# Performance work log

Hardware: AMD Instinct MI355X
Metric: run time of the kernel (lower is better)

The kernel has to match this reference:

```python
import jax, jax.numpy as jnp
import numpy as np

MASK_FILL = -987654321.0


def rotate_every_two(x):
    # pairs (x0, x1) -> (-x1, x0), interleaved back along last dim
    x1 = x[..., 0::2]
    x2 = x[..., 1::2]
    return jnp.stack((-x2, x1), axis=-1).reshape(x.shape)


def setup_inputs() -> dict:
    key = jax.random.key(0)
    ks = jax.random.split(key, 6)
    b, n, dim = 64, 197, 768
    heads, dim_head = 12, 64
    inner = heads * dim_head
    x = jax.random.normal(ks[0], (b, n, dim), dtype=jnp.float32)
    pos_emb = jax.random.normal(ks[1], (1, n, dim_head), dtype=jnp.float32)
    w_qkv = jax.random.normal(ks[2], (dim, 3 * inner), dtype=jnp.float32) * (dim ** -0.5)
    scale = jnp.full((heads,), dim_head ** -0.5, dtype=jnp.float32)
    w_out = jax.random.normal(ks[3], (inner, dim), dtype=jnp.float32) * (inner ** -0.5)
    b_out = jnp.zeros((dim,), dtype=jnp.float32)
    return {"x": x, "pos_emb": pos_emb, "w_qkv": w_qkv, "scale": scale,
            "w_out": w_out, "b_out": b_out}


def reference(x, pos_emb, w_qkv, scale, w_out, b_out):
    b, n, dim = x.shape
    h = scale.shape[0]
    qkv = x @ w_qkv                         # [b, n, 3*inner]
    q, k, v = jnp.split(qkv, 3, axis=-1)
    dh = q.shape[-1] // h
    to_heads = lambda t: t.reshape(b, n, h, dh).transpose(0, 2, 1, 3)  # bhnd
    q, k, v = to_heads(q), to_heads(k), to_heads(v)

    # RoPE: pos_emb [1, n, (2 * dh/2)] -> sin/cos [n, dh/2] -> interleave to [n, dh]
    sc = pos_emb[0].reshape(n, 2, dh // 2)
    sin = jnp.repeat(sc[:, 0], 2, axis=-1)  # [n, dh]
    cos = jnp.repeat(sc[:, 1], 2, axis=-1)
    q = q * cos + rotate_every_two(q) * sin
    k = k * cos + rotate_every_two(k) * sin

    # per-head learnable scale
    dots = jnp.einsum('bhid,bhjd->bhij', q, k) * scale[None, :, None, None]
    # diagonal (LSA) mask
    eye = jnp.eye(n, dtype=bool)
    dots = jnp.where(eye, MASK_FILL, dots)

    attn = jax.nn.softmax(dots, axis=-1)
    out = jnp.einsum('bhij,bhjd->bhid', attn, v)
    out = out.transpose(0, 2, 1, 3).reshape(b, n, h * dh)
    return out @ w_out + b_out
```

## Files before the change

kernel.cpp:

```cpp
#include <hip/hip_runtime.h>
#include <math.h>

#define MASK_FILL_F (-987654321.0f)

typedef unsigned short u16;
typedef unsigned int   u32;

constexpr int Bb   = 64;
constexpr int Ntok = 197;
constexpr int Dim  = 768;
constexpr int Heads= 12;
constexpr int Dh   = 64;
constexpr int Nq3  = 2304;
constexpr int Rows = 12608;
constexpr int Mpad = 12672;

using f32x4  = __attribute__((ext_vector_type(4))) float;
using bf16x8 = __attribute__((ext_vector_type(8))) short;

__device__ __forceinline__ u16 f2bf(float f) {
  u32 u = __float_as_uint(f);
  u = (u + 0x7fffu + ((u >> 16) & 1u)) >> 16;
  return (u16)u;
}

__device__ __forceinline__ void stage16(const void* gp, void* lp) {
  __builtin_amdgcn_global_load_lds(
      (const __attribute__((address_space(1))) u32*)gp,
      (__attribute__((address_space(3))) u32*)lp, 16, 0, 0);
}

__device__ __forceinline__ int sigma6(int M) {
  return (M & 0x23) | (((M >> 3) & 1) << 4) | (((M >> 2) & 1) << 3) |
         (((M >> 4) & 1) << 2);
}

constexpr int NB_CVT = (Rows * Dim / 4 + 255) / 256;
constexpr int NB_TQ  = (Nq3 / 32) * (Dim / 32);
constexpr int NB_TO  = (Dim / 32) * (Dim / 32);

__global__ __launch_bounds__(256) void prep(
    const float* __restrict__ x, u16* __restrict__ xb,
    const float* __restrict__ w_qkv, u16* __restrict__ wqkvT,
    const float* __restrict__ w_out, u16* __restrict__ woutT)
{
  __shared__ float t[32][33];
  const int bid = blockIdx.x, tid = threadIdx.x;

  if (bid < NB_CVT) {
    const int i = bid * 256 + tid;
    if (i < Rows * Dim / 4) {
      const float4 v = *(const float4*)&x[(size_t)i * 4];
      ushort4 u;
      u.x = f2bf(v.x); u.y = f2bf(v.y); u.z = f2bf(v.z); u.w = f2bf(v.w);
      *(ushort4*)&xb[(size_t)i * 4] = u;
    }
    return;
  }

  const float* in; u16* out; int R, C, c0, r0;
  if (bid < NB_CVT + NB_TQ) {
    const int b2 = bid - NB_CVT;
    in = w_qkv; out = wqkvT; R = Dim; C = Nq3;
    c0 = (b2 % (Nq3 / 32)) * 32; r0 = (b2 / (Nq3 / 32)) * 32;
  } else {
    const int b3 = bid - NB_CVT - NB_TQ;
    in = w_out; out = woutT; R = Dim; C = Dim;
    c0 = (b3 % (Dim / 32)) * 32; r0 = (b3 / (Dim / 32)) * 32;
  }
  const int tx = tid & 31, ty = tid >> 5;
#pragma unroll
  for (int rr = ty; rr < 32; rr += 8)
    t[rr][tx] = in[(size_t)(r0 + rr) * C + c0 + tx];
  __syncthreads();
#pragma unroll
  for (int cc = ty; cc < 32; cc += 8)
    out[(size_t)(c0 + cc) * R + r0 + tx] = f2bf(t[tx][cc]);
}

constexpr int Kc  = 768;
constexpr int NKT = Kc / 64;
#define KTC(x) ((x) < NKT ? (x) : (NKT - 1))

#define BARM()  asm volatile("s_barrier" ::: "memory")
#define VMW4()  asm volatile("s_waitcnt vmcnt(4)" ::: "memory")
#define LGKM0() asm volatile("s_waitcnt lgkmcnt(0)" ::: "memory")

#define STGA(chunk, kt, BUF) \
  stage16(Ag + (size_t)(m0 + (chunk) * 8 + srow) * Kc + (kt) * 64 + scol, \
          &As[BUF][(chunk) * 512])
#define STGB(chunk, kt, BUF) \
  stage16(Bg + (size_t)(n0 + (chunk) * 8 + srow) * Kc + (kt) * 64 + scol, \
          &Bs[BUF][(chunk) * 512])

#define RDA(BUF, MH) \
  _Pragma("unroll") for (int m_ = 0; m_ < 4; ++m_) \
  _Pragma("unroll") for (int k_ = 0; k_ < 2; ++k_) \
    af[m_][k_] = *(const bf16x8*)&As[BUF][(wr * 128 + (MH) * 64 + m_ * 16 + tx) * 64 \
                                          + (((k_ * 4 + qd) ^ sx) * 8)];
#define RDB(BUF, NH, BFR) \
  _Pragma("unroll") for (int n_ = 0; n_ < 2; ++n_) \
  _Pragma("unroll") for (int k_ = 0; k_ < 2; ++k_) \
    BFR[n_][k_] = *(const bf16x8*)&Bs[BUF][(wc * 64 + (NH) * 32 + n_ * 16 + tx) * 64 \
                                           + (((k_ * 4 + qd) ^ sx) * 8)];

#define MM(MH, NH, BFR) \
  __builtin_amdgcn_s_setprio(1); \
  _Pragma("unroll") for (int m_ = 0; m_ < 4; ++m_) \
  _Pragma("unroll") for (int n_ = 0; n_ < 2; ++n_) \
  _Pragma("unroll") for (int k_ = 0; k_ < 2; ++k_) \
    acc[(MH) * 4 + m_][(NH) * 2 + n_] = __builtin_amdgcn_mfma_f32_16x16x32_bf16( \
        af[m_][k_], BFR[n_][k_], acc[(MH) * 4 + m_][(NH) * 2 + n_], 0, 0, 0); \
  __builtin_amdgcn_s_setprio(0);

template<int TN>
__global__ __launch_bounds__(512, 2) void gemm8p(
    const u16* __restrict__ Ag, const u16* __restrict__ Bg,
    u16* __restrict__ Cb, int Nn, int nwg,
    const float* __restrict__ pe)
{
  __shared__ u16 As[2][256 * 64];
  __shared__ u16 Bs[2][256 * 64];

  const int tid = threadIdx.x, lane = tid & 63, w = tid >> 6;

  const int orig = blockIdx.x;
  const int q8 = nwg >> 3, r8 = nwg & 7;
  const int xcd = orig & 7, sub = orig >> 3;
  const int wgid = (xcd < r8 ? xcd * (q8 + 1) : r8 * (q8 + 1) + (xcd - r8) * q8) + sub;
  const int tm = wgid / TN, tn = wgid % TN;
  const int m0 = tm * 256, n0 = tn * 256;

  const int wr = w >> 2, wc = w & 3;
  const int tx = lane & 15, qd = lane >> 4, sx = tx & 7;

  const int srow = lane >> 3;
  const int scol = ((lane & 7) ^ srow) * 8;
  const int b0 = (w >> 1) * 8 + (w & 1) * 2;

  STGA(w, 0, 0);        STGA(16 + w, 0, 0);
  STGB(b0 + 4, 0, 0);   STGB(b0 + 5, 0, 0);
  STGA(8 + w, 0, 0);    STGA(24 + w, 0, 0);
  STGB(b0, 0, 0);       STGB(b0 + 1, 0, 0);
  STGA(w, 1, 1);        STGA(16 + w, 1, 1);
  STGB(b0 + 4, 1, 1);   STGB(b0 + 5, 1, 1);
  VMW4();
  BARM();

  f32x4  acc[8][4] = {};
  bf16x8 af[4][2], bf0[2][2], bf1[2][2];

#pragma unroll 1
  for (int i = 0; i < NKT / 2; ++i) {
    const int u = 2 * i;
    RDA(0, 0); RDB(0, 0, bf0); RDB(0, 1, bf1);
    STGA(8 + w, u + 1, 1); STGA(24 + w, u + 1, 1);
    STGB(b0, u + 1, 1);    STGB(b0 + 1, u + 1, 1);
    LGKM0(); BARM();
    MM(0, 0, bf0); MM(0, 1, bf1);
    RDA(0, 1);
    STGA(w, KTC(u + 2), 0);      STGA(16 + w, KTC(u + 2), 0);
    STGB(b0 + 4, KTC(u + 2), 0); STGB(b0 + 5, KTC(u + 2), 0);
    LGKM0(); VMW4(); BARM();
    MM(1, 1, bf1); MM(1, 0, bf0);
    RDA(1, 0); RDB(1, 0, bf0); RDB(1, 1, bf1);
    STGA(8 + w, KTC(u + 2), 0); STGA(24 + w, KTC(u + 2), 0);
    STGB(b0, KTC(u + 2), 0);    STGB(b0 + 1, KTC(u + 2), 0);
    LGKM0(); BARM();
    MM(0, 0, bf0); MM(0, 1, bf1);
    RDA(1, 1);
    STGA(w, KTC(u + 3), 1);      STGA(16 + w, KTC(u + 3), 1);
    STGB(b0 + 4, KTC(u + 3), 1); STGB(b0 + 5, KTC(u + 3), 1);
    LGKM0(); VMW4(); BARM();
    MM(1, 1, bf1); MM(1, 0, bf0);
  }

  const bool dorot = (n0 < 2 * Dim);
#pragma unroll
  for (int mi = 0; mi < 8; ++mi) {
    const int rbase = m0 + wr * 128 + mi * 16 + qd * 4;
    int iq[4];
#pragma unroll
    for (int r = 0; r < 4; ++r) iq[r] = (rbase + r) % Ntok;
#pragma unroll
    for (int ni = 0; ni < 4; ++ni) {
      const int col = n0 + wc * 64 + ni * 16 + tx;
      const int mm  = (col & 63) >> 1;
      const int odd = col & 1;
#pragma unroll
      for (int r = 0; r < 4; ++r) {
        float v = acc[mi][ni][r];
        float res = v;
        if (dorot) {
          const float other = __shfl_xor(v, 1, 64);
          const float sn = pe[iq[r] * 64 + mm];
          const float c2 = pe[iq[r] * 64 + 32 + mm];
          res = odd ? (v * c2 + other * sn) : (v * c2 - other * sn);
        }
        Cb[(size_t)(rbase + r) * Nn + col] = f2bf(res);
      }
    }
  }
}

__global__ __launch_bounds__(256) void gemm_bt1(
    const u16* __restrict__ Ag, const u16* __restrict__ Bg,
    float* __restrict__ C, int K, int Nn, const float* __restrict__ bias)
{
  __shared__ u16 As[128 * 32];
  __shared__ u16 Bs[128 * 32];
  const int tid = threadIdx.x, lane = tid & 63, w = tid >> 6;
  const int m0 = blockIdx.y * 128, n0 = blockIdx.x * 128;
  const int wm = (w & 1) * 64, wn = (w >> 1) * 64;
  const int tx = lane & 15, qk = lane >> 4;
  const int rs = lane >> 2, cs = (lane & 3) * 8;

  f32x4 acc[4][4] = {};

  for (int k0 = 0; k0 < K; k0 += 32) {
#pragma unroll
    for (int t = 0; t < 2; ++t) {
      const int r0 = w * 16 + t * 64;
      stage16(Ag + (size_t)(m0 + r0 + rs) * K + k0 + cs, &As[r0 * 32]);
      stage16(Bg + (size_t)(n0 + r0 + rs) * K + k0 + cs, &Bs[r0 * 32]);
    }
    __syncthreads();
    bf16x8 af[4], bf[4];
#pragma unroll
    for (int f = 0; f < 4; ++f) {
      af[f] = *(const bf16x8*)&As[(wm + f * 16 + tx) * 32 + qk * 8];
      bf[f] = *(const bf16x8*)&Bs[(wn + f * 16 + tx) * 32 + qk * 8];
    }
#pragma unroll
    for (int fm = 0; fm < 4; ++fm)
#pragma unroll
      for (int fn = 0; fn < 4; ++fn)
        acc[fm][fn] = __builtin_amdgcn_mfma_f32_16x16x32_bf16(
            af[fm], bf[fn], acc[fm][fn], 0, 0, 0);
    __syncthreads();
  }

#pragma unroll
  for (int fm = 0; fm < 4; ++fm) {
    const int rbase = m0 + wm + fm * 16 + qk * 4;
#pragma unroll
    for (int fn = 0; fn < 4; ++fn) {
      const int col = n0 + wn + fn * 16 + tx;
      const float bv = bias[col];
#pragma unroll
      for (int r = 0; r < 4; ++r) {
        const int row = rbase + r;
        if (row < Rows) C[(size_t)row * Nn + col] = acc[fm][fn][r] + bv;
      }
    }
  }
}

constexpr int LS = 72;

__global__ __launch_bounds__(1024) void attn16(
    const u16* __restrict__ qkvB,
    const float* __restrict__ scale, u16* __restrict__ outB)
{
  __shared__ u16 ks  [64 * LS];
  __shared__ u16 vtmp[64 * LS];
  __shared__ u16 vts [64 * LS];

  const int bh = blockIdx.x;
  const int b = bh / Heads, h = bh % Heads;
  const float sc = scale[h];
  const int tid = threadIdx.x, lane = tid & 63, w = tid >> 6;
  const int tx = lane & 15, q = lane >> 4;
  const size_t rowbase = (size_t)b * Ntok;
  const bool active = (w < 13);

  const int Ms = (tid & 511) >> 3, c8s = (tid & 7) * 8;
  const bool isK = tid < 512;
  const u16* kgp = qkvB + (rowbase + sigma6(Ms)) * (size_t)Nq3 + Dim + h * Dh + c8s;
  const u16* vgp = qkvB + (rowbase + Ms) * (size_t)Nq3 + 2 * Dim + h * Dh + c8s;
  u16* slds = (isK ? ks : vtmp) + Ms * LS + c8s;

  const int td = tid & 63, tj8 = (tid & 511) >> 6;

  bf16x8 bq[2];
  if (active) {
#pragma unroll
    for (int kk = 0; kk < 2; ++kk)
      bq[kk] = *(const bf16x8*)(qkvB +
          (rowbase + 16 * w + tx) * (size_t)Nq3 + h * Dh + kk * 32 + q * 8);
  }

  uint4 sreg = isK ? *(const uint4*)kgp : *(const uint4*)vgp;

  float l_part = 0.f;
  f32x4 oacc[4] = {};

  for (int jt = 0; jt < 4; ++jt) {
    const int j0 = jt * 64;
    __syncthreads();
    *(uint4*)slds = sreg;
    __syncthreads();

    if (!isK) {
      if (jt < 3) {
        const int j = (jt + 1) * 64 + Ms;
        sreg = (j < Ntok) ? *(const uint4*)(vgp + (size_t)(jt + 1) * 64 * Nq3)
                          : make_uint4(0u, 0u, 0u, 0u);
      }
    } else {
      ushort4 lo, hi;
      lo.x = vtmp[(tj8 * 8 + 0) * LS + td]; lo.y = vtmp[(tj8 * 8 + 1) * LS + td];
      lo.z = vtmp[(tj8 * 8 + 2) * LS + td]; lo.w = vtmp[(tj8 * 8 + 3) * LS + td];
      hi.x = vtmp[(tj8 * 8 + 4) * LS + td]; hi.y = vtmp[(tj8 * 8 + 5) * LS + td];
      hi.z = vtmp[(tj8 * 8 + 6) * LS + td]; hi.w = vtmp[(tj8 * 8 + 7) * LS + td];
      *(ushort4*)&vts[td * LS + tj8 * 8]     = lo;
      *(ushort4*)&vts[td * LS + tj8 * 8 + 4] = hi;
      if (jt < 3)
        sreg = *(const uint4*)(kgp + (size_t)(jt + 1) * 64 * Nq3);
    }
    __syncthreads();

    if (active) {
      f32x4 sT[4] = {};
      __builtin_amdgcn_s_setprio(1);
#pragma unroll
      for (int kk = 0; kk < 2; ++kk)
#pragma unroll
        for (int jb = 0; jb < 4; ++jb) {
          const bf16x8 ka = *(const bf16x8*)&ks[(jb * 16 + tx) * LS + kk * 32 + q * 8];
          sT[jb] = __builtin_amdgcn_mfma_f32_16x16x32_bf16(ka, bq[kk], sT[jb], 0, 0, 0);
        }
      __builtin_amdgcn_s_setprio(0);

      const int ig = 16 * w + tx;
      union { bf16x8 v; u16 e[8]; } pk[2];
      float lp = 0.f;
#pragma unroll
      for (int jb = 0; jb < 4; ++jb)
#pragma unroll
        for (int r = 0; r < 4; ++r) {
          const int jg = j0 + 32 * (jb >> 1) + 8 * q + 4 * (jb & 1) + r;
          const float s = fminf(sT[jb][r] * sc, 80.f);
          const bool bad = (jg >= Ntok) || (jg == ig);
          const float p = bad ? 0.f : __expf(s);
          lp += p;
          pk[jb >> 1].e[(jb & 1) * 4 + r] = f2bf(p);
        }
      l_part += lp;

      __builtin_amdgcn_s_setprio(1);
#pragma unroll
      for (int kk = 0; kk < 2; ++kk)
#pragma unroll
        for (int nb = 0; nb < 4; ++nb) {
          const bf16x8 vb = *(const bf16x8*)&vts[(nb * 16 + tx) * LS + kk * 32 + q * 8];
          oacc[nb] = __builtin_amdgcn_mfma_f32_16x16x32_bf16(pk[kk].v, vb,
                                                            oacc[nb], 0, 0, 0);
        }
      __builtin_amdgcn_s_setprio(0);
    }
  }

  if (active) {
    float l = l_part;
    l += __shfl_xor(l, 16, 64);
    l += __shfl_xor(l, 32, 64);
    const float linv = 1.0f / l;
#pragma unroll
    for (int r = 0; r < 4; ++r) {
      const float lr = __shfl(linv, 4 * q + r, 64);
      const int igr = 16 * w + 4 * q + r;
      if (igr < Ntok) {
#pragma unroll
        for (int nb = 0; nb < 4; ++nb)
          outB[(rowbase + igr) * (size_t)Dim + h * Dh + nb * 16 + tx] =
              f2bf(oacc[nb][r] * lr);
      }
    }
  }
}

extern "C" void kernel_launch(void* const* d_in, const int* in_sizes, int n_in,
                              void* d_out, int out_size, void* d_ws, size_t ws_size,
                              hipStream_t stream) {
  const float* x     = (const float*)d_in[0];
  const float* pe    = (const float*)d_in[1];
  const float* w_qkv = (const float*)d_in[2];
  const float* scale = (const float*)d_in[3];
  const float* w_out = (const float*)d_in[4];
  const float* b_out = (const float*)d_in[5];
  float* out = (float*)d_out;

  u16* xb    = (u16*)d_ws;
  u16* wqkvT = xb    + (size_t)Mpad * Dim;
  u16* woutT = wqkvT + (size_t)Nq3 * Dim;
  u16* qkvB  = woutT + (size_t)Dim * Dim;
  u16* attnB = qkvB  + (size_t)Mpad * Nq3;

  prep<<<NB_CVT + NB_TQ + NB_TO, 256, 0, stream>>>(x, xb, w_qkv, wqkvT, w_out, woutT);

  constexpr int NWG0 = 50 * 9;
  gemm8p<9><<<NWG0, 512, 0, stream>>>(xb, wqkvT, qkvB, Nq3, NWG0, pe);

  attn16<<<Bb * Heads, 1024, 0, stream>>>(qkvB, scale, attnB);

  gemm_bt1<<<dim3(Dim / 128, Mpad / 128), 256, 0, stream>>>(
      attnB, woutT, out, Dim, Dim, b_out);
}
```

Before: 254.5 us.

## Replace output projection GEMM with double-buffered swizzled XCD-remapped pipelined kernel

```diff
diff --git a/kernel.cpp b/kernel.cpp
--- a/kernel.cpp
+++ b/kernel.cpp
@@ -203,54 +203,104 @@
   }
 }
 
-__global__ __launch_bounds__(256) void gemm_bt1(
+#define STGA1(chunk, kt, BUF) \
+  stage16(Ag + (size_t)(m0 + (chunk) * 8 + srow) * Kc + (kt) * 64 + scol, \
+          &As[BUF][(chunk) * 512])
+#define STGB1(chunk, kt, BUF) \
+  stage16(Bg + (size_t)(n0 + (chunk) * 8 + srow) * Kc + (kt) * 64 + scol, \
+          &Bs[BUF][(chunk) * 512])
+
+#define RDA1(BUF, MH) \
+  _Pragma("unroll") for (int m_ = 0; m_ < 2; ++m_) \
+  _Pragma("unroll") for (int k_ = 0; k_ < 2; ++k_) \
+    af[m_][k_] = *(const bf16x8*)&As[BUF][(wr * 64 + (MH) * 32 + m_ * 16 + tx) * 64 \
+                                          + (((k_ * 4 + qd) ^ sx) * 8)];
+#define RDB1(BUF, NH, BFR) \
+  _Pragma("unroll") for (int n_ = 0; n_ < 2; ++n_) \
+  _Pragma("unroll") for (int k_ = 0; k_ < 2; ++k_) \
+    BFR[n_][k_] = *(const bf16x8*)&Bs[BUF][(wc * 64 + (NH) * 32 + n_ * 16 + tx) * 64 \
+                                           + (((k_ * 4 + qd) ^ sx) * 8)];
+
+#define MM1(MH, NH, BFR) \
+  __builtin_amdgcn_s_setprio(1); \
+  _Pragma("unroll") for (int m_ = 0; m_ < 2; ++m_) \
+  _Pragma("unroll") for (int n_ = 0; n_ < 2; ++n_) \
+  _Pragma("unroll") for (int k_ = 0; k_ < 2; ++k_) \
+    acc[(MH) * 2 + m_][(NH) * 2 + n_] = __builtin_amdgcn_mfma_f32_16x16x32_bf16( \
+        af[m_][k_], BFR[n_][k_], acc[(MH) * 2 + m_][(NH) * 2 + n_], 0, 0, 0); \
+  __builtin_amdgcn_s_setprio(0);
+
+template<int TN>
+__global__ __launch_bounds__(256, 2) void gemm1m(
     const u16* __restrict__ Ag, const u16* __restrict__ Bg,
-    float* __restrict__ C, int K, int Nn, const float* __restrict__ bias)
+    float* __restrict__ C, int Nn, int nwg, const float* __restrict__ bias)
 {
-  __shared__ u16 As[128 * 32];
-  __shared__ u16 Bs[128 * 32];
+  __shared__ u16 As[2][128 * 64];
+  __shared__ u16 Bs[2][128 * 64];
+
   const int tid = threadIdx.x, lane = tid & 63, w = tid >> 6;
-  const int m0 = blockIdx.y * 128, n0 = blockIdx.x * 128;
-  const int wm = (w & 1) * 64, wn = (w >> 1) * 64;
-  const int tx = lane & 15, qk = lane >> 4;
-  const int rs = lane >> 2, cs = (lane & 3) * 8;
-
-  f32x4 acc[4][4] = {};
-
-  for (int k0 = 0; k0 < K; k0 += 32) {
-#pragma unroll
-    for (int t = 0; t < 2; ++t) {
-      const int r0 = w * 16 + t * 64;
-      stage16(Ag + (size_t)(m0 + r0 + rs) * K + k0 + cs, &As[r0 * 32]);
-      stage16(Bg + (size_t)(n0 + r0 + rs) * K + k0 + cs, &Bs[r0 * 32]);
-    }
-    __syncthreads();
-    bf16x8 af[4], bf[4];
-#pragma unroll
-    for (int f = 0; f < 4; ++f) {
-      af[f] = *(const bf16x8*)&As[(wm + f * 16 + tx) * 32 + qk * 8];
-      bf[f] = *(const bf16x8*)&Bs[(wn + f * 16 + tx) * 32 + qk * 8];
-    }
-#pragma unroll
-    for (int fm = 0; fm < 4; ++fm)
-#pragma unroll
-      for (int fn = 0; fn < 4; ++fn)
-        acc[fm][fn] = __builtin_amdgcn_mfma_f32_16x16x32_bf16(
-            af[fm], bf[fn], acc[fm][fn], 0, 0, 0);
-    __syncthreads();
-  }
-
-#pragma unroll
-  for (int fm = 0; fm < 4; ++fm) {
-    const int rbase = m0 + wm + fm * 16 + qk * 4;
-#pragma unroll
-    for (int fn = 0; fn < 4; ++fn) {
-      const int col = n0 + wn + fn * 16 + tx;
+
+  const int orig = blockIdx.x;
+  const int q8 = nwg >> 3, r8 = nwg & 7;
+  const int xcd = orig & 7, sub = orig >> 3;
+  const int wgid = (xcd < r8 ? xcd * (q8 + 1) : r8 * (q8 + 1) + (xcd - r8) * q8) + sub;
+  const int tm = wgid / TN, tn = wgid % TN;
+  const int m0 = tm * 128, n0 = tn * 128;
+
+  const int wr = w >> 1, wc = w & 1;
+  const int tx = lane & 15, qd = lane >> 4, sx = tx & 7;
+
+  const int srow = lane >> 3;
+  const int scol = ((lane & 7) ^ srow) * 8;
+
+  STGA1(w, 0, 0);       STGA1(8 + w, 0, 0);
+  STGB1(4 + w, 0, 0);   STGB1(12 + w, 0, 0);
+  STGA1(4 + w, 0, 0);   STGA1(12 + w, 0, 0);
+  STGB1(w, 0, 0);       STGB1(8 + w, 0, 0);
+  STGA1(w, 1, 1);       STGA1(8 + w, 1, 1);
+  STGB1(4 + w, 1, 1);   STGB1(12 + w, 1, 1);
+  VMW4();
+  BARM();
+
+  f32x4  acc[4][4] = {};
+  bf16x8 af[2][2], bf0[2][2], bf1[2][2];
+
+#pragma unroll 1
+  for (int i = 0; i < NKT / 2; ++i) {
+    const int u = 2 * i;
+    RDA1(0, 0); RDB1(0, 0, bf0); RDB1(0, 1, bf1);
+    STGA1(4 + w, u + 1, 1); STGA1(12 + w, u + 1, 1);
+    STGB1(w, u + 1, 1);     STGB1(8 + w, u + 1, 1);
+    LGKM0(); BARM();
+    MM1(0, 0, bf0); MM1(0, 1, bf1);
+    RDA1(0, 1);
+    STGA1(w, KTC(u + 2), 0);     STGA1(8 + w, KTC(u + 2), 0);
+    STGB1(4 + w, KTC(u + 2), 0); STGB1(12 + w, KTC(u + 2), 0);
+    LGKM0(); VMW4(); BARM();
+    MM1(1, 1, bf1); MM1(1, 0, bf0);
+    RDA1(1, 0); RDB1(1, 0, bf0); RDB1(1, 1, bf1);
+    STGA1(4 + w, KTC(u + 2), 0); STGA1(12 + w, KTC(u + 2), 0);
+    STGB1(w, KTC(u + 2), 0);     STGB1(8 + w, KTC(u + 2), 0);
+    LGKM0(); BARM();
+    MM1(0, 0, bf0); MM1(0, 1, bf1);
+    RDA1(1, 1);
+    STGA1(w, KTC(u + 3), 1);     STGA1(8 + w, KTC(u + 3), 1);
+    STGB1(4 + w, KTC(u + 3), 1); STGB1(12 + w, KTC(u + 3), 1);
+    LGKM0(); VMW4(); BARM();
+    MM1(1, 1, bf1); MM1(1, 0, bf0);
+  }
+
+#pragma unroll
+  for (int mi = 0; mi < 4; ++mi) {
+    const int rbase = m0 + wr * 64 + mi * 16 + qd * 4;
+#pragma unroll
+    for (int ni = 0; ni < 4; ++ni) {
+      const int col = n0 + wc * 64 + ni * 16 + tx;
       const float bv = bias[col];
 #pragma unroll
       for (int r = 0; r < 4; ++r) {
         const int row = rbase + r;
-        if (row < Rows) C[(size_t)row * Nn + col] = acc[fm][fn][r] + bv;
+        if (row < Rows) C[(size_t)row * Nn + col] = acc[mi][ni][r] + bv;
       }
     }
   }
@@ -404,6 +454,6 @@
 
   attn16<<<Bb * Heads, 1024, 0, stream>>>(qkvB, scale, attnB);
 
-  gemm_bt1<<<dim3(Dim / 128, Mpad / 128), 256, 0, stream>>>(
-      attnB, woutT, out, Dim, Dim, b_out);
-}
+  constexpr int NWG1 = 100 * 6;
+  gemm1m<6><<<NWG1, 256, 0, stream>>>(attnB, woutT, out, Dim, NWG1, b_out);
+}
```

New measurement: 258.0 us. No clear change (+1.3%).
